# Kernel optimization log

Hardware: AMD Instinct MI355X
Metric: run time of the kernel (lower is better)

The kernel has to match this reference:

```python
import jax, jax.numpy as jnp
from jax import lax
import numpy as np

E = 3            # num_experts
HEAD_CONV = 128  # head_conv
N_HEADS = 3      # hm, wh, reg
HEAD_CH = 2      # channels per head
BN_EPS = 1e-5


def _conv(x, w, stride, pad, groups=1):
    return lax.conv_general_dilated(
        x, w, (stride, stride), [(pad, pad), (pad, pad)],
        feature_group_count=groups,
        dimension_numbers=('NCHW', 'OIHW', 'NCHW'))


def _maxpool3s2p1(x):
    return lax.reduce_window(
        x, -jnp.inf, lax.max, (1, 1, 3, 3), (1, 1, 2, 2),
        ((0, 0), (0, 0), (1, 1), (1, 1)))


def setup_inputs() -> dict:
    key = jax.random.key(0)
    ks = jax.random.split(key, 8)
    B, C, T, H, W = 16, 3, 5, 384, 384
    s = 0.05
    inp = {
        'x': jax.random.normal(ks[0], (B, C, T, H, W), jnp.float32),
        # gating network params
        'g_conv_w': jax.random.normal(ks[1], (64, C * T, 7, 7), jnp.float32) * s,
        'g_bn_gamma': jnp.ones((64,), jnp.float32),
        'g_bn_beta': jnp.zeros((64,), jnp.float32),
        'g_bn_mean': jnp.zeros((64,), jnp.float32),
        'g_bn_var': jnp.ones((64,), jnp.float32),
        'g_fc_w': jax.random.normal(ks[2], (E, 64), jnp.float32) * s,
        'g_fc_b': jnp.zeros((E,), jnp.float32),
        # frozen expert params (stacked over expert dim E)
        'e_conv1_w': jax.random.normal(ks[3], (E, 64, C * T, 7, 7), jnp.float32) * s,
        'e_conv1_b': jnp.zeros((E, 64), jnp.float32),
        'e_head_w1': jax.random.normal(ks[4], (E, N_HEADS * HEAD_CONV, 64, 3, 3), jnp.float32) * s,
        'e_head_b1': jnp.zeros((E, N_HEADS * HEAD_CONV), jnp.float32),
        'e_head_w2': jax.random.normal(ks[5], (E, N_HEADS * HEAD_CH, HEAD_CONV, 1, 1), jnp.float32) * s,
        'e_head_b2': jnp.zeros((E, N_HEADS * HEAD_CH), jnp.float32),
    }
    return inp


def reference(x, g_conv_w, g_bn_gamma, g_bn_beta, g_bn_mean, g_bn_var,
              g_fc_w, g_fc_b, e_conv1_w, e_conv1_b,
              e_head_w1, e_head_b1, e_head_w2, e_head_b2):
    b, c, t, h, w = x.shape
    xr = x.reshape(b, c * t, h, w)

    # ---- ConvGatingNetwork ----
    f = _conv(xr, g_conv_w, 2, 3)                                  # [B,64,H/2,W/2]
    inv = g_bn_gamma / jnp.sqrt(g_bn_var + BN_EPS)
    f = f * inv[None, :, None, None] + (g_bn_beta - g_bn_mean * inv)[None, :, None, None]
    f = jax.nn.relu(f)
    f = _maxpool3s2p1(f)                                           # [B,64,H/4,W/4]
    feat = f.mean(axis=(2, 3))                                     # [B,64]
    logits = feat @ g_fc_w.T + g_fc_b                              # [B,E]
    idx = jnp.argmax(logits, axis=1)                               # top-1
    onehot = jax.nn.one_hot(idx, E, dtype=logits.dtype)            # [B,E]
    density = onehot.mean(axis=0)
    density_proxy = jax.nn.softmax(logits, axis=1).mean(axis=0)
    aux_loss = (density * density_proxy).sum() * E

    # ---- Experts (frozen DSFNet stand-in), computed densely then gathered ----
    def expert(cw, cb, hw1, hb1, hw2, hb2):
        y = jax.nn.relu(_conv(xr, cw, 4, 3) + cb[None, :, None, None])       # [B,64,H/4,W/4]
        y = jax.nn.relu(_conv(y, hw1, 1, 1) + hb1[None, :, None, None])      # [B,384,h,w]
        y = _conv(y, hw2, 1, 0, groups=N_HEADS) + hb2[None, :, None, None]   # [B,6,h,w]
        return y

    out_all = jax.vmap(expert)(e_conv1_w, e_conv1_b, e_head_w1, e_head_b1,
                               e_head_w2, e_head_b2)               # [E,B,6,h,w]
    out_all = lax.stop_gradient(out_all)  # experts frozen + torch.no_grad
    out = jnp.einsum('be,ebchw->bchw', onehot, out_all)            # per-sample top-1 gather
    return out, 0.01 * aux_loss
```

## Files before the change

kernel.cpp:

```cpp
#include <hip/hip_runtime.h>
#include <math.h>

#define BB 16
#define CIN 15
#define HW 384
#define XPL 147456
#define NX 35389440
#define PH 96
#define GW 192
#define YP 98
#define Y1IPL (98*98*64)
#define OUT_ELEMS (BB*6*PH*PH)

#define OFF_WG   0
#define OFF_WE1  122880
#define OFF_WH   491520
#define OFF_GSH  1818624
#define OFF_FEAT 1818880
#define OFF_IDX  1822976
#define OFF_CBUF 2097152

typedef __attribute__((ext_vector_type(8))) short short8;
typedef __attribute__((ext_vector_type(4))) float floatx4;
typedef __attribute__((ext_vector_type(4))) unsigned int uintx4;
typedef __attribute__((ext_vector_type(2))) unsigned int uintx2;

__device__ __forceinline__ unsigned bf16rne(float f) {
  unsigned u = __float_as_uint(f);
  unsigned r = ((u >> 16) & 1u) + 0x7FFFu;
  return (u + r) >> 16;
}
__device__ __forceinline__ float bf2f(unsigned short s) {
  return __uint_as_float(((unsigned)s) << 16);
}

__global__ __launch_bounds__(256) void k_prep(
    const float* __restrict__ g_conv_w, const float* __restrict__ e_conv1_w,
    const float* __restrict__ e_head_w1,
    const float* __restrict__ gamma, const float* __restrict__ var,
    const float* __restrict__ beta,  const float* __restrict__ mean,
    unsigned char* __restrict__ wsb)
{
  int i = blockIdx.x * 256 + threadIdx.x;
  unsigned short* Wg  = (unsigned short*)(wsb + OFF_WG);
  unsigned short* We1 = (unsigned short*)(wsb + OFF_WE1);
  unsigned short* Wh  = (unsigned short*)(wsb + OFF_WH);
  float* gsh = (float*)(wsb + OFF_GSH);
  if (i < 61440) {
    int j = i & 7, lane = (i >> 3) & 63, mtc = i >> 9;
    int mt = mtc & 3, c = mtc >> 2, ic = c >> 1, h = c & 1;
    int oc = mt * 16 + (lane & 15), q = lane >> 4;
    int ky = 4 * h + q, kx = j;
    float v = 0.f;
    if (ky < 7 && kx < 7) v = g_conv_w[oc * 735 + ic * 49 + ky * 7 + kx];
    float inv = gamma[oc] * rsqrtf(var[oc] + 1e-5f);
    Wg[i] = (unsigned short)bf16rne(v * inv);
  } else if (i < 245760) {
    int r = i - 61440;
    int e = r / 61440, r2 = r % 61440;
    int j = r2 & 7, lane = (r2 >> 3) & 63, mtc = r2 >> 9;
    int mt = mtc & 3, c = mtc >> 2, ic = c >> 1, h = c & 1;
    int oc = mt * 16 + (lane & 15), q = lane >> 4;
    int ky = 4 * h + q, kx = j;
    float v = 0.f;
    if (ky < 7 && kx < 7) v = e_conv1_w[(e * 64 + oc) * 735 + ic * 49 + ky * 7 + kx];
    We1[r] = (unsigned short)bf16rne(v);
  } else if (i < 909312) {
    int r = i - 245760;
    int e = r / 221184, r2 = r % 221184;
    int j = r2 & 7, lane = (r2 >> 3) & 63, mtc = r2 >> 9;
    int mt = mtc % 24, chunk = mtc / 24;
    int kk = chunk >> 1, ih = chunk & 1;
    int oc = mt * 16 + (lane & 15), q = lane >> 4;
    int ic = ih * 32 + q * 8 + j;
    Wh[r] = (unsigned short)bf16rne(e_head_w1[((e * 384 + oc) * 64 + ic) * 9 + kk]);
  } else if (i < 909376) {
    int oc = i - 909312;
    float inv = gamma[oc] * rsqrtf(var[oc] + 1e-5f);
    gsh[oc] = beta[oc] - mean[oc] * inv;
  }
}

__global__ __launch_bounds__(256) void k_gconv(
    const float* __restrict__ x, const unsigned short* __restrict__ Wg,
    const float* __restrict__ gsh, unsigned short* __restrict__ Cbuf)
{
  const int t = threadIdx.x, w = t >> 6, lane = t & 63, q = lane >> 4, ln = lane & 15;
  const int px0 = blockIdx.x * 16, py0 = blockIdx.y * 16, b = blockIdx.z;
  const int iy0 = 2 * py0 - 3, ix0 = 2 * px0 - 3;

  __shared__ unsigned tilU[11400];

  {
    const bool edge = (blockIdx.x == 0) | (blockIdx.x == 11) |
                      (blockIdx.y == 0) | (blockIdx.y == 11);
    const int xbase = b * CIN * XPL;
    if (!edge) {
      for (int it = 0; it < 5; ++it) {
        int i = it * 256 + t;
        if (i < 1140) {
          int half = i & 1, ri = i >> 1;
          int ic = ri / 38, row = ri - ic * 38;
          int iy = iy0 + row;
          int A = ix0 + 20 * half - 1;
          const float* src = x + xbase + ic * XPL + iy * HW + A;
          floatx4 F[6];
#pragma unroll
          for (int s = 0; s < 6; ++s) F[s] = *(const floatx4*)(src + 4 * s);
          float f[24];
#pragma unroll
          for (int s = 0; s < 6; ++s) {
            f[4*s] = F[s].x; f[4*s+1] = F[s].y; f[4*s+2] = F[s].z; f[4*s+3] = F[s].w;
          }
          unsigned* dst = tilU + ic * 760 + row * 20 + 10 * half;
#pragma unroll
          for (int jj = 0; jj < 5; ++jj) {
            uintx2 pr;
            pr.x = bf16rne(f[1 + 4*jj]) | (bf16rne(f[2 + 4*jj]) << 16);
            pr.y = bf16rne(f[3 + 4*jj]) | (bf16rne(f[4 + 4*jj]) << 16);
            *(uintx2*)(dst + 2 * jj) = pr;
          }
        }
      }
    } else {
      for (int it = 0; it < 5; ++it) {
        int i = it * 256 + t;
        if (i < 1140) {
          int half = i & 1, ri = i >> 1;
          int ic = ri / 38, row = ri - ic * 38;
          int iy = iy0 + row;
          unsigned rowm = (iy >= 0 && iy < HW) ? 0xFFFFFFFFu : 0u;
          int A = ix0 + 20 * half - 1;
          int a = xbase + ic * XPL + iy * HW + A;
          floatx4 F[6];
#pragma unroll
          for (int s = 0; s < 6; ++s) {
            int as = a + 4 * s;
            as = max(as, 0); as = min(as, NX - 4);
            F[s] = *(const floatx4*)(x + as);
          }
          float f[24];
#pragma unroll
          for (int s = 0; s < 6; ++s) {
            f[4*s] = F[s].x; f[4*s+1] = F[s].y; f[4*s+2] = F[s].z; f[4*s+3] = F[s].w;
          }
          unsigned* dst = tilU + ic * 760 + row * 20 + 10 * half;
#pragma unroll
          for (int jj = 0; jj < 5; ++jj) {
            uintx2 pr;
#pragma unroll
            for (int k = 0; k < 2; ++k) {
              int j = 2 * jj + k;
              int c = A + 1 + 2 * j;
              unsigned m = rowm;
              m &= ((c >= 0) && (c < HW)) ? 0xFFFFFFFFu : 0xFFFF0000u;
              m &= ((c + 1 >= 0) && (c + 1 < HW)) ? 0xFFFFFFFFu : 0x0000FFFFu;
              unsigned d = (bf16rne(f[1 + 2*j]) | (bf16rne(f[2 + 2*j]) << 16)) & m;
              if (k == 0) pr.x = d; else pr.y = d;
            }
            *(uintx2*)(dst + 2 * jj) = pr;
          }
        }
      }
    }
  }
  __syncthreads();

  floatx4 acc[4][4];
#pragma unroll
  for (int mt = 0; mt < 4; ++mt)
#pragma unroll
    for (int nt = 0; nt < 4; ++nt) acc[mt][nt] = 0.f;

#pragma unroll 3
  for (int ic = 0; ic < CIN; ++ic) {
#pragma unroll
    for (int h = 0; h < 2; ++h) {
      short8 af[4];
#pragma unroll
      for (int mt = 0; mt < 4; ++mt)
        af[mt] = *(const short8*)(Wg + (((ic * 2 + h) * 4 + mt) << 9) + lane * 8);
      short8 bf[4];
#pragma unroll
      for (int nt = 0; nt < 4; ++nt) {
        int row = 2 * (w * 4 + nt) + 4 * h + q;
        int bd = ic * 760 + row * 20 + ln;
        union { unsigned u[4]; short8 s; } cv;
        cv.u[0] = tilU[bd]; cv.u[1] = tilU[bd + 1];
        cv.u[2] = tilU[bd + 2]; cv.u[3] = tilU[bd + 3];
        bf[nt] = cv.s;
      }
#pragma unroll
      for (int mt = 0; mt < 4; ++mt)
#pragma unroll
        for (int nt = 0; nt < 4; ++nt)
          acc[mt][nt] = __builtin_amdgcn_mfma_f32_16x16x32_bf16(af[mt], bf[nt], acc[mt][nt], 0, 0, 0);
    }
  }

#pragma unroll
  for (int nt = 0; nt < 4; ++nt) {
    int py = py0 + w * 4 + nt, px = px0 + ln;
    size_t rowo = (((size_t)b * GW + py) * GW + px) * 64;
#pragma unroll
    for (int mt = 0; mt < 4; ++mt) {
      int ocb = mt * 16 + q * 4;
      float v0 = fmaxf(acc[mt][nt][0] + gsh[ocb + 0], 0.f);
      float v1 = fmaxf(acc[mt][nt][1] + gsh[ocb + 1], 0.f);
      float v2 = fmaxf(acc[mt][nt][2] + gsh[ocb + 2], 0.f);
      float v3 = fmaxf(acc[mt][nt][3] + gsh[ocb + 3], 0.f);
      uintx2 pr;
      pr.x = (bf16rne(v1) << 16) | bf16rne(v0);
      pr.y = (bf16rne(v3) << 16) | bf16rne(v2);
      *(uintx2*)(Cbuf + rowo + ocb) = pr;
    }
  }
}

__global__ __launch_bounds__(256) void k_pool(const unsigned short* __restrict__ Cb,
                                              float* __restrict__ feat)
{
  const int py = blockIdx.x, b = blockIdx.y;
  const int t = threadIdx.x, oc = t & 63, strip = t >> 6;
  const unsigned short* base = Cb + (size_t)b * GW * GW * 64 + oc;
  float sum = 0.f;
  for (int px = strip * 24; px < strip * 24 + 24; ++px) {
    float m = 0.f;
#pragma unroll
    for (int dy = 0; dy < 3; ++dy) {
      int row = 2 * py - 1 + dy;
      if (row < 0 || row >= GW) continue;
#pragma unroll
      for (int dx = 0; dx < 3; ++dx) {
        int col = 2 * px - 1 + dx;
        if (col < 0 || col >= GW) continue;
        m = fmaxf(m, bf2f(base[((size_t)row * GW + col) * 64]));
      }
    }
    sum += m;
  }
  __shared__ float red[4][64];
  red[strip][oc] = sum;
  __syncthreads();
  if (t < 64) {
    float s = red[0][oc] + red[1][oc] + red[2][oc] + red[3][oc];
    atomicAdd(&feat[b * 64 + oc], s);
  }
}

__global__ __launch_bounds__(64) void k_gate_fc(
    const float* __restrict__ feat, const float* __restrict__ fcw,
    const float* __restrict__ fcb, int* __restrict__ idxb,
    float* __restrict__ out_aux)
{
  __shared__ float sm[16][3];
  __shared__ int sidx[16];
  int t = threadIdx.x;
  if (t < 16) {
    float l[3];
#pragma unroll
    for (int e = 0; e < 3; ++e) {
      float s = fcb[e];
      for (int c = 0; c < 64; ++c)
        s = fmaf(feat[t * 64 + c] * (1.f / 9216.f), fcw[e * 64 + c], s);
      l[e] = s;
    }
    int best = 0; float bv = l[0];
    if (l[1] > bv) { bv = l[1]; best = 1; }
    if (l[2] > bv) { bv = l[2]; best = 2; }
    sidx[t] = best; idxb[t] = best;
    float mx = fmaxf(l[0], fmaxf(l[1], l[2]));
    float e0 = expf(l[0] - mx), e1 = expf(l[1] - mx), e2 = expf(l[2] - mx);
    float d = e0 + e1 + e2;
    sm[t][0] = e0 / d; sm[t][1] = e1 / d; sm[t][2] = e2 / d;
  }
  __syncthreads();
  if (t == 0) {
    float aux = 0.f;
    for (int e = 0; e < 3; ++e) {
      float cnt = 0.f, pr = 0.f;
      for (int b = 0; b < 16; ++b) { cnt += (sidx[b] == e) ? 1.f : 0.f; pr += sm[b][e]; }
      aux += (cnt / 16.f) * (pr / 16.f);
    }
    *out_aux = 0.01f * aux * 3.f;
  }
}

__global__ __launch_bounds__(256) void k_econv(
    const float* __restrict__ x, const unsigned short* __restrict__ We1,
    const float* __restrict__ biasp, const int* __restrict__ idxb,
    unsigned short* __restrict__ Y1)
{
  const int t = threadIdx.x, w = t >> 6, lane = t & 63, q = lane >> 4, ln = lane & 15;
  const int b = blockIdx.z;
  const int e = idxb[b];
  const unsigned short* W = We1 + e * 61440;
  const float* bs = biasp + e * 64;
  const int px0 = blockIdx.x * 16, py0 = blockIdx.y * 16;
  const int px = px0 + ln;

  const int c0 = 4 * px - 3;
  const int acol = c0 - 1;
  unsigned pm[4];
#pragma unroll
  for (int j = 0; j < 4; ++j) {
    int t0 = 2 * j, t1 = 2 * j + 1;
    unsigned m0 = (c0 + t0 >= 0 && c0 + t0 < HW) ? 0x0000FFFFu : 0u;
    unsigned m1 = (c0 + t1 >= 0 && c0 + t1 < HW) ? 0xFFFF0000u : 0u;
    pm[j] = m0 | m1;
  }

  int syq[4];
#pragma unroll
  for (int nt = 0; nt < 4; ++nt) syq[nt] = 4 * (py0 + w * 4 + nt) + q - 3;
  const int xbase = b * CIN * XPL;

  floatx4 acc[4][4];
#pragma unroll
  for (int mt = 0; mt < 4; ++mt)
#pragma unroll
    for (int nt = 0; nt < 4; ++nt) acc[mt][nt] = 0.f;

#pragma unroll 3
  for (int ic = 0; ic < CIN; ++ic) {
    const int icb = xbase + ic * XPL;
#pragma unroll
    for (int h = 0; h < 2; ++h) {
      short8 af[4];
#pragma unroll
      for (int mt = 0; mt < 4; ++mt)
        af[mt] = *(const short8*)(W + (((ic * 2 + h) * 4 + mt) << 9) + lane * 8);
      short8 bf[4];
#pragma unroll
      for (int nt = 0; nt < 4; ++nt) {
        int iy = syq[nt] + 4 * h;
        bool rv = (iy >= 0) && (iy < HW) && ((4 * h + q) < 7);
        int a0 = icb + iy * HW + acol;
        a0 = max(a0, 0); a0 = min(a0, NX - 12);
        const float* fp = x + a0;
        floatx4 fA = *(const floatx4*)(fp);
        floatx4 fB = *(const floatx4*)(fp + 4);
        floatx4 fC = *(const floatx4*)(fp + 8);
        float g[8];
        g[0] = fA.y; g[1] = fA.z; g[2] = fA.w; g[3] = fB.x;
        g[4] = fB.y; g[5] = fB.z; g[6] = fB.w; g[7] = fC.x;
        union { unsigned u[4]; short8 s; } cv;
#pragma unroll
        for (int j = 0; j < 4; ++j) {
          unsigned p = __builtin_amdgcn_perm(__float_as_uint(g[2 * j + 1]),
                                             __float_as_uint(g[2 * j]), 0x07060302u);
          p &= pm[j];
          cv.u[j] = rv ? p : 0u;
        }
        bf[nt] = cv.s;
      }
#pragma unroll
      for (int mt = 0; mt < 4; ++mt)
#pragma unroll
        for (int nt = 0; nt < 4; ++nt)
          acc[mt][nt] = __builtin_amdgcn_mfma_f32_16x16x32_bf16(af[mt], bf[nt], acc[mt][nt], 0, 0, 0);
    }
  }

#pragma unroll
  for (int nt = 0; nt < 4; ++nt) {
    int py = py0 + w * 4 + nt;
    size_t rowo = (((size_t)b * YP + py + 1) * YP + px + 1) * 64;
#pragma unroll
    for (int mt = 0; mt < 4; ++mt) {
      int ocb = mt * 16 + q * 4;
      float v0 = fmaxf(acc[mt][nt][0] + bs[ocb + 0], 0.f);
      float v1 = fmaxf(acc[mt][nt][1] + bs[ocb + 1], 0.f);
      float v2 = fmaxf(acc[mt][nt][2] + bs[ocb + 2], 0.f);
      float v3 = fmaxf(acc[mt][nt][3] + bs[ocb + 3], 0.f);
      uintx2 pr;
      pr.x = (bf16rne(v1) << 16) | bf16rne(v0);
      pr.y = (bf16rne(v3) << 16) | bf16rne(v2);
      *(uintx2*)(Y1 + rowo + ocb) = pr;
    }
  }
}

__global__ __launch_bounds__(768, 3) void k_headm(
    const unsigned short* __restrict__ Y1, const unsigned short* __restrict__ Whp,
    const float* __restrict__ b1, const float* __restrict__ w2,
    const float* __restrict__ b2, const int* __restrict__ idxb,
    float* __restrict__ out)
{
  const int t = threadIdx.x, w = t >> 6, lane = t & 63, q = lane >> 4, ln = lane & 15;
  const int wo = w & 3, wn = w >> 2;
  const int b = blockIdx.z, px0 = blockIdx.x * 16, py0 = blockIdx.y * 6;
  const int e = idxb[b];
  const unsigned short* W = Whp + e * 221184;

  __shared__ unsigned short patch[8 * 18 * 72];
  __shared__ float sred[6][4][16][6];

  {
    uintx4 vv[2];
#pragma unroll
    for (int r = 0; r < 2; ++r) {
      int i = r * 768 + t;
      if (i < 1152) {
        int row = i / 144, rem = i % 144, col = rem >> 3, s = rem & 7;
        vv[r] = *(const uintx4*)(Y1 + (((size_t)b * YP + py0 + row) * YP + (px0 + col)) * 64 + s * 8);
      }
    }
#pragma unroll
    for (int r = 0; r < 2; ++r) {
      int i = r * 768 + t;
      if (i < 1152) {
        int row = i / 144, rem = i % 144, col = rem >> 3, s = rem & 7;
        *(uintx4*)(patch + (row * 18 + col) * 72 + s * 8) = vv[r];
      }
    }
  }
  __syncthreads();

  floatx4 acc[6][2];
#pragma unroll
  for (int mt = 0; mt < 6; ++mt)
#pragma unroll
    for (int j = 0; j < 2; ++j) acc[mt][j] = 0.f;

#pragma unroll
  for (int kk = 0; kk < 9; ++kk) {
    const int ky = kk / 3, kx = kk % 3;
#pragma unroll
    for (int ih = 0; ih < 2; ++ih) {
      short8 bf[2];
#pragma unroll
      for (int j = 0; j < 2; ++j) {
        int nt = wn * 2 + j;
        int off = ((nt + ky) * 18 + (ln + kx)) * 72 + ih * 32 + q * 8;
        bf[j] = *(const short8*)(patch + off);
      }
      const int cbase = ((kk * 2 + ih) * 24 + wo * 6) << 9;
#pragma unroll
      for (int mt = 0; mt < 6; ++mt) {
        short8 af = *(const short8*)(W + cbase + (mt << 9) + lane * 8);
#pragma unroll
        for (int j = 0; j < 2; ++j)
          acc[mt][j] = __builtin_amdgcn_mfma_f32_16x16x32_bf16(af, bf[j], acc[mt][j], 0, 0, 0);
      }
    }
  }

#pragma unroll
  for (int j = 0; j < 2; ++j) {
    const int nt = wn * 2 + j;
    float part[6] = {0.f, 0.f, 0.f, 0.f, 0.f, 0.f};
#pragma unroll
    for (int mt = 0; mt < 6; ++mt) {
      int ocb = wo * 96 + mt * 16 + q * 4;
#pragma unroll
      for (int r = 0; r < 4; ++r) {
        int oc = ocb + r;
        float y = fmaxf(acc[mt][j][r] + b1[e * 384 + oc], 0.f);
        int g = oc >> 7, kb = oc & 127;
        part[2 * g]     += y * w2[(e * 6 + 2 * g) * 128 + kb];
        part[2 * g + 1] += y * w2[(e * 6 + 2 * g + 1) * 128 + kb];
      }
    }
#pragma unroll
    for (int c = 0; c < 6; ++c) {
      part[c] += __shfl_down(part[c], 32);
      part[c] += __shfl_down(part[c], 16);
    }
    if (q == 0) {
#pragma unroll
      for (int c = 0; c < 6; ++c) sred[nt][wo][ln][c] = part[c];
    }
  }
  __syncthreads();
  if (t < 576) {
    int pix = t / 6, c = t % 6;
    int nt = pix >> 4, pl = pix & 15;
    float s = sred[nt][0][pl][c] + sred[nt][1][pl][c] + sred[nt][2][pl][c] +
              sred[nt][3][pl][c] + b2[e * 6 + c];
    out[(((size_t)(b * 6 + c)) * PH + (py0 + nt)) * PH + (px0 + pl)] = s;
  }
}

extern "C" void kernel_launch(void* const* d_in, const int* in_sizes, int n_in,
                              void* d_out, int out_size, void* d_ws, size_t ws_size,
                              hipStream_t stream)
{
  const float* x         = (const float*)d_in[0];
  const float* g_fc_w    = (const float*)d_in[6];
  const float* g_fc_b    = (const float*)d_in[7];
  const float* e_conv1_b = (const float*)d_in[9];
  const float* e_head_b1 = (const float*)d_in[11];
  const float* e_head_w2 = (const float*)d_in[12];
  const float* e_head_b2 = (const float*)d_in[13];

  unsigned char* wsb = (unsigned char*)d_ws;
  unsigned short* Wg  = (unsigned short*)(wsb + OFF_WG);
  unsigned short* We1 = (unsigned short*)(wsb + OFF_WE1);
  unsigned short* Wh  = (unsigned short*)(wsb + OFF_WH);
  float* gsh  = (float*)(wsb + OFF_GSH);
  float* feat = (float*)(wsb + OFF_FEAT);
  int*   idxb = (int*)(wsb + OFF_IDX);
  unsigned short* Cbuf = (unsigned short*)(wsb + OFF_CBUF);
  unsigned short* Y1   = (unsigned short*)(wsb + OFF_CBUF);

  float* out = (float*)d_out;
  float* out_aux = out + OUT_ELEMS;

  hipMemsetAsync(feat, 0, 16 * 64 * sizeof(float), stream);
  hipLaunchKernelGGL(k_prep, dim3(3553), dim3(256), 0, stream,
                     (const float*)d_in[1], (const float*)d_in[8], (const float*)d_in[10],
                     (const float*)d_in[2], (const float*)d_in[5],
                     (const float*)d_in[3], (const float*)d_in[4], wsb);

  hipLaunchKernelGGL(k_gconv, dim3(12, 12, 16), dim3(256), 0, stream,
                     x, Wg, gsh, Cbuf);
  hipLaunchKernelGGL(k_pool, dim3(96, 16), dim3(256), 0, stream, Cbuf, feat);
  hipLaunchKernelGGL(k_gate_fc, dim3(1), dim3(64), 0, stream,
                     feat, g_fc_w, g_fc_b, idxb, out_aux);

  hipMemsetAsync(Y1, 0, (size_t)BB * Y1IPL * 2, stream);
  hipLaunchKernelGGL(k_econv, dim3(6, 6, 16), dim3(256), 0, stream,
                     x, We1, e_conv1_b, idxb, Y1);

  hipLaunchKernelGGL(k_headm, dim3(6, 16, 16), dim3(768), 0, stream,
                     Y1, Wh, e_head_b1, e_head_w2, e_head_b2, idxb, out);
}
```

Measured before the change: 621.8 us.

## Double-buffer gating conv input tiles, remap blocks, and zero only Y1 halo ring

The gating conv kernel now stages its input three channels at a time into a double-buffered shared tile. Global loads for the next chunk are issued before the MFMA work on the current chunk, so load latency overlaps compute. Shared memory shrinks, which allows the 3-blocks-per-SM launch bound. Blocks are also reordered with a linear remap, and the full memset of the padded Y1 buffer is replaced by a small kernel that zeroes only the one-pixel border ring, on the assumption that k_econv writes every interior element.

Measured after the change: 611.5 us. About the same (-1.6%).

```diff
diff --git a/kernel.cpp b/kernel.cpp
--- a/kernel.cpp
+++ b/kernel.cpp
@@ -81,121 +81,128 @@
   }
 }
 
-__global__ __launch_bounds__(256) void k_gconv(
+__global__ __launch_bounds__(256, 3) void k_gconv(
     const float* __restrict__ x, const unsigned short* __restrict__ Wg,
     const float* __restrict__ gsh, unsigned short* __restrict__ Cbuf)
 {
   const int t = threadIdx.x, w = t >> 6, lane = t & 63, q = lane >> 4, ln = lane & 15;
-  const int px0 = blockIdx.x * 16, py0 = blockIdx.y * 16, b = blockIdx.z;
+
+  int lin = blockIdx.x + 12 * (blockIdx.y + 12 * blockIdx.z);
+  int nl = (lin & 7) * 288 + (lin >> 3);
+  const int b = nl / 144; int r144 = nl - b * 144;
+  const int by = r144 / 12, bx = r144 - by * 12;
+
+  const int px0 = bx * 16, py0 = by * 16;
   const int iy0 = 2 * py0 - 3, ix0 = 2 * px0 - 3;
-
-  __shared__ unsigned tilU[11400];
-
-  {
-    const bool edge = (blockIdx.x == 0) | (blockIdx.x == 11) |
-                      (blockIdx.y == 0) | (blockIdx.y == 11);
-    const int xbase = b * CIN * XPL;
+  const bool edge = (bx == 0) | (bx == 11) | (by == 0) | (by == 11);
+  const int xbase = b * CIN * XPL;
+
+  __shared__ unsigned tilU[2][2280];
+
+  const bool act = (t < 228);
+  const int lic = t / 76, r2 = t - lic * 76, srow = r2 >> 1, half = r2 & 1;
+  const int iy = iy0 + srow;
+  const int A = ix0 + 20 * half - 1;
+  const unsigned rowm = (iy >= 0 && iy < HW) ? 0xFFFFFFFFu : 0u;
+  const int abase = xbase + iy * HW + A;
+  const int dloc = (lic * 38 + srow) * 20 + 10 * half;
+
+  floatx4 F[6];
+
+  auto issue = [&](int c) {
+    if (!act) return;
+    int a = abase + (c * 3 + lic) * XPL;
     if (!edge) {
-      for (int it = 0; it < 5; ++it) {
-        int i = it * 256 + t;
-        if (i < 1140) {
-          int half = i & 1, ri = i >> 1;
-          int ic = ri / 38, row = ri - ic * 38;
-          int iy = iy0 + row;
-          int A = ix0 + 20 * half - 1;
-          const float* src = x + xbase + ic * XPL + iy * HW + A;
-          floatx4 F[6];
-#pragma unroll
-          for (int s = 0; s < 6; ++s) F[s] = *(const floatx4*)(src + 4 * s);
-          float f[24];
-#pragma unroll
-          for (int s = 0; s < 6; ++s) {
-            f[4*s] = F[s].x; f[4*s+1] = F[s].y; f[4*s+2] = F[s].z; f[4*s+3] = F[s].w;
-          }
-          unsigned* dst = tilU + ic * 760 + row * 20 + 10 * half;
-#pragma unroll
-          for (int jj = 0; jj < 5; ++jj) {
-            uintx2 pr;
-            pr.x = bf16rne(f[1 + 4*jj]) | (bf16rne(f[2 + 4*jj]) << 16);
-            pr.y = bf16rne(f[3 + 4*jj]) | (bf16rne(f[4 + 4*jj]) << 16);
-            *(uintx2*)(dst + 2 * jj) = pr;
-          }
+      const float* src = x + a;
+#pragma unroll
+      for (int s = 0; s < 6; ++s) F[s] = *(const floatx4*)(src + 4 * s);
+    } else {
+#pragma unroll
+      for (int s = 0; s < 6; ++s) {
+        int as = a + 4 * s;
+        as = max(as, 0); as = min(as, NX - 4);
+        F[s] = *(const floatx4*)(x + as);
+      }
+    }
+  };
+
+  auto commit = [&](unsigned* buf) {
+    if (!act) return;
+    float f[24];
+#pragma unroll
+    for (int s = 0; s < 6; ++s) {
+      f[4*s] = F[s].x; f[4*s+1] = F[s].y; f[4*s+2] = F[s].z; f[4*s+3] = F[s].w;
+    }
+    unsigned* dst = buf + dloc;
+    if (!edge) {
+#pragma unroll
+      for (int jj = 0; jj < 5; ++jj) {
+        uintx2 pr;
+        pr.x = bf16rne(f[1 + 4*jj]) | (bf16rne(f[2 + 4*jj]) << 16);
+        pr.y = bf16rne(f[3 + 4*jj]) | (bf16rne(f[4 + 4*jj]) << 16);
+        *(uintx2*)(dst + 2 * jj) = pr;
+      }
+    } else {
+#pragma unroll
+      for (int jj = 0; jj < 5; ++jj) {
+        uintx2 pr;
+#pragma unroll
+        for (int k = 0; k < 2; ++k) {
+          int j = 2 * jj + k;
+          int cc = A + 1 + 2 * j;
+          unsigned m = rowm;
+          m &= ((cc >= 0) && (cc < HW)) ? 0xFFFFFFFFu : 0xFFFF0000u;
+          m &= ((cc + 1 >= 0) && (cc + 1 < HW)) ? 0xFFFFFFFFu : 0x0000FFFFu;
+          unsigned d = (bf16rne(f[1 + 2*j]) | (bf16rne(f[2 + 2*j]) << 16)) & m;
+          if (k == 0) pr.x = d; else pr.y = d;
         }
-      }
-    } else {
-      for (int it = 0; it < 5; ++it) {
-        int i = it * 256 + t;
-        if (i < 1140) {
-          int half = i & 1, ri = i >> 1;
-          int ic = ri / 38, row = ri - ic * 38;
-          int iy = iy0 + row;
-          unsigned rowm = (iy >= 0 && iy < HW) ? 0xFFFFFFFFu : 0u;
-          int A = ix0 + 20 * half - 1;
-          int a = xbase + ic * XPL + iy * HW + A;
-          floatx4 F[6];
-#pragma unroll
-          for (int s = 0; s < 6; ++s) {
-            int as = a + 4 * s;
-            as = max(as, 0); as = min(as, NX - 4);
-            F[s] = *(const floatx4*)(x + as);
-          }
-          float f[24];
-#pragma unroll
-          for (int s = 0; s < 6; ++s) {
-            f[4*s] = F[s].x; f[4*s+1] = F[s].y; f[4*s+2] = F[s].z; f[4*s+3] = F[s].w;
-          }
-          unsigned* dst = tilU + ic * 760 + row * 20 + 10 * half;
-#pragma unroll
-          for (int jj = 0; jj < 5; ++jj) {
-            uintx2 pr;
-#pragma unroll
-            for (int k = 0; k < 2; ++k) {
-              int j = 2 * jj + k;
-              int c = A + 1 + 2 * j;
-              unsigned m = rowm;
-              m &= ((c >= 0) && (c < HW)) ? 0xFFFFFFFFu : 0xFFFF0000u;
-              m &= ((c + 1 >= 0) && (c + 1 < HW)) ? 0xFFFFFFFFu : 0x0000FFFFu;
-              unsigned d = (bf16rne(f[1 + 2*j]) | (bf16rne(f[2 + 2*j]) << 16)) & m;
-              if (k == 0) pr.x = d; else pr.y = d;
-            }
-            *(uintx2*)(dst + 2 * jj) = pr;
-          }
+        *(uintx2*)(dst + 2 * jj) = pr;
+      }
+    }
+  };
+
+  floatx4 acc[4][4];
+#pragma unroll
+  for (int mt = 0; mt < 4; ++mt)
+#pragma unroll
+    for (int nt = 0; nt < 4; ++nt) acc[mt][nt] = 0.f;
+
+  issue(0);
+  commit(tilU[0]);
+  __syncthreads();
+
+#pragma unroll 1
+  for (int c = 0; c < 5; ++c) {
+    if (c < 4) issue(c + 1);
+    const unsigned* buf = tilU[c & 1];
+#pragma unroll
+    for (int l2 = 0; l2 < 3; ++l2) {
+      const int ic = c * 3 + l2;
+#pragma unroll
+      for (int h = 0; h < 2; ++h) {
+        short8 af[4];
+#pragma unroll
+        for (int mt = 0; mt < 4; ++mt)
+          af[mt] = *(const short8*)(Wg + (((ic * 2 + h) * 4 + mt) << 9) + lane * 8);
+        short8 bfv[4];
+#pragma unroll
+        for (int nt = 0; nt < 4; ++nt) {
+          int rrow = 2 * (w * 4 + nt) + 4 * h + q;
+          int bd = l2 * 760 + rrow * 20 + ln;
+          union { unsigned u[4]; short8 s; } cv;
+          cv.u[0] = buf[bd]; cv.u[1] = buf[bd + 1];
+          cv.u[2] = buf[bd + 2]; cv.u[3] = buf[bd + 3];
+          bfv[nt] = cv.s;
         }
-      }
-    }
-  }
-  __syncthreads();
-
-  floatx4 acc[4][4];
-#pragma unroll
-  for (int mt = 0; mt < 4; ++mt)
-#pragma unroll
-    for (int nt = 0; nt < 4; ++nt) acc[mt][nt] = 0.f;
-
-#pragma unroll 3
-  for (int ic = 0; ic < CIN; ++ic) {
-#pragma unroll
-    for (int h = 0; h < 2; ++h) {
-      short8 af[4];
-#pragma unroll
-      for (int mt = 0; mt < 4; ++mt)
-        af[mt] = *(const short8*)(Wg + (((ic * 2 + h) * 4 + mt) << 9) + lane * 8);
-      short8 bf[4];
-#pragma unroll
-      for (int nt = 0; nt < 4; ++nt) {
-        int row = 2 * (w * 4 + nt) + 4 * h + q;
-        int bd = ic * 760 + row * 20 + ln;
-        union { unsigned u[4]; short8 s; } cv;
-        cv.u[0] = tilU[bd]; cv.u[1] = tilU[bd + 1];
-        cv.u[2] = tilU[bd + 2]; cv.u[3] = tilU[bd + 3];
-        bf[nt] = cv.s;
-      }
-#pragma unroll
-      for (int mt = 0; mt < 4; ++mt)
-#pragma unroll
-        for (int nt = 0; nt < 4; ++nt)
-          acc[mt][nt] = __builtin_amdgcn_mfma_f32_16x16x32_bf16(af[mt], bf[nt], acc[mt][nt], 0, 0, 0);
-    }
+#pragma unroll
+        for (int mt = 0; mt < 4; ++mt)
+#pragma unroll
+          for (int nt = 0; nt < 4; ++nt)
+            acc[mt][nt] = __builtin_amdgcn_mfma_f32_16x16x32_bf16(af[mt], bfv[nt], acc[mt][nt], 0, 0, 0);
+      }
+    }
+    if (c < 4) commit(tilU[(c + 1) & 1]);
+    __syncthreads();
   }
 
 #pragma unroll
@@ -283,6 +290,29 @@
       aux += (cnt / 16.f) * (pr / 16.f);
     }
     *out_aux = 0.01f * aux * 3.f;
+  }
+}
+
+__global__ __launch_bounds__(256) void k_zring(unsigned short* __restrict__ Y1)
+{
+  const int b = blockIdx.x, t = threadIdx.x;
+  uintx4* Yv = (uintx4*)Y1;
+  uintx4 z = 0;
+  for (int i = t; i < 3104; i += 256) {
+    int v;
+    if (i < 784) {
+      v = (b * YP + 0) * 784 + i;
+    } else if (i < 1568) {
+      v = (b * YP + 97) * 784 + (i - 784);
+    } else {
+      int j = i - 1568;
+      int colg = j / 768;
+      int jj = j - colg * 768;
+      int col = colg ? 97 : 0;
+      int rr = 1 + (jj >> 3);
+      v = (b * YP + rr) * 784 + col * 8 + (jj & 7);
+    }
+    Yv[v] = z;
   }
 }
 
@@ -519,7 +549,7 @@
   hipLaunchKernelGGL(k_gate_fc, dim3(1), dim3(64), 0, stream,
                      feat, g_fc_w, g_fc_b, idxb, out_aux);
 
-  hipMemsetAsync(Y1, 0, (size_t)BB * Y1IPL * 2, stream);
+  hipLaunchKernelGGL(k_zring, dim3(16), dim3(256), 0, stream, Y1);
   hipLaunchKernelGGL(k_econv, dim3(6, 6, 16), dim3(256), 0, stream,
                      x, We1, e_conv1_b, idxb, Y1);
 
```
